# Kernel optimization log

Measured on AMD Instinct MI355X. Metric: run time of the kernel, lower is better.

The kernel has to match this reference:

```python
import jax, jax.numpy as jnp
import numpy as np
import math

N_EMBD = 1024
NUM_HEADS = 16
MAX_LEN = 2048
AUX = 256
B, T = 2, 2048


def setup_inputs() -> dict:
    key = jax.random.key(0)
    ks = jax.random.split(key, 16)
    s = 0.02
    C, A = N_EMBD, AUX
    inp = {
        "x": jax.random.normal(ks[0], (B, T, C), jnp.float32),
        "aux_x": jax.random.normal(ks[1], (B, T, A), jnp.float32),
        "Wq": s * jax.random.normal(ks[2], (C, C), jnp.float32),
        "bq": jnp.zeros((C,), jnp.float32),
        "Wk": s * jax.random.normal(ks[3], (C + A, C), jnp.float32),
        "bk": jnp.zeros((C,), jnp.float32),
        "Wv": s * jax.random.normal(ks[4], (C + A, C), jnp.float32),
        "bv": jnp.zeros((C,), jnp.float32),
        "Wo": s * jax.random.normal(ks[5], (C, C), jnp.float32),  # zero-init in source; randomized for a meaningful baseline
        "bo": jnp.zeros((C,), jnp.float32),
        "PEq": s * jax.random.normal(ks[6], (MAX_LEN, C), jnp.float32),
        "PEk": s * jax.random.normal(ks[7], (MAX_LEN, C), jnp.float32),
        "attn_mask": jax.random.bernoulli(ks[8], 0.9, (B, T, T)),
        "frame_indices": jax.random.randint(ks[9], (B, T), 0, MAX_LEN),
        "num_heads": NUM_HEADS,
    }
    return inp


def reference(x, aux_x, Wq, bq, Wk, bk, Wv, bv, Wo, bo, PEq, PEk, attn_mask, frame_indices, num_heads):
    Bx, Tx, C = x.shape
    H = num_heads
    hd = C // H
    x_aug = jnp.concatenate([x, aux_x], axis=2)  # [B,T,C+A]
    # QKV projections, split heads; PE added per (position, head) to q and k
    q = (x @ Wq + bq).reshape(Bx, Tx, H, hd) + PEq[frame_indices].reshape(Bx, Tx, H, hd)
    k = (x_aug @ Wk + bk).reshape(Bx, Tx, H, hd) + PEk[frame_indices].reshape(Bx, Tx, H, hd)
    v = (x_aug @ Wv + bv).reshape(Bx, Tx, H, hd)
    scale = 1.0 / math.sqrt(hd)
    scores = jnp.einsum("bqhd,bkhd->bhqk", q, k) * scale  # [B,H,T,T]
    scores = jnp.where(attn_mask[:, None, :, :], scores, -jnp.inf)
    attn = jax.nn.softmax(scores, axis=-1)  # fully-masked rows -> NaN
    out = jnp.einsum("bhqk,bkhd->bqhd", attn, v).reshape(Bx, Tx, C)
    out = jnp.nan_to_num(out, nan=0.0)
    return out @ Wo + bo
```

## Files before the change

### kernel.cpp

```cpp
#include <hip/hip_runtime.h>
#include <hip/hip_bf16.h>

typedef unsigned short u16;
typedef unsigned int u32;
typedef __attribute__((ext_vector_type(8))) short bf16x8;
typedef __attribute__((ext_vector_type(4))) float f32x4;

#define HD 64
#define NH 16
#define TT 2048
#define BB 2
#define CA 1280

__device__ __forceinline__ u16 bfu(float f) {
    u32 u = __builtin_bit_cast(u32, f);
    u32 r = u + 0x7fffu + ((u >> 16) & 1u);
    return (u16)(r >> 16);
}

__device__ __forceinline__ float ex2(float x) {
#if __has_builtin(__builtin_amdgcn_exp2f)
    return __builtin_amdgcn_exp2f(x);
#else
    return exp2f(x);
#endif
}

__device__ __forceinline__ void gload16(const void* g, void* l) {
    __builtin_amdgcn_global_load_lds(
        (const __attribute__((address_space(1))) unsigned int*)g,
        (__attribute__((address_space(3))) unsigned int*)l,
        16, 0, 0);
}

__global__ void build_xaug(const float* __restrict__ x, const float* __restrict__ aux,
                           u16* __restrict__ xa) {
    int i = blockIdx.x * 256 + threadIdx.x;
    int row = i / 320;
    int c4 = i - row * 320;
    float4 v;
    if (c4 < 256) v = ((const float4*)x)[row * 256 + c4];
    else          v = ((const float4*)aux)[row * 64 + (c4 - 256)];
    u16 o0 = bfu(v.x), o1 = bfu(v.y), o2 = bfu(v.z), o3 = bfu(v.w);
    ushort4 pk; pk.x = o0; pk.y = o1; pk.z = o2; pk.w = o3;
    ((ushort4*)xa)[i] = pk;
}

__global__ void wtrans_all(const float* __restrict__ Wq, const float* __restrict__ Wk,
                           const float* __restrict__ Wv, const float* __restrict__ Wo,
                           u16* __restrict__ WTall, u16* __restrict__ WTo) {
    int z = blockIdx.z;
    const float* src = (z == 0) ? Wq : (z == 1) ? Wk : (z == 2) ? Wv : Wo;
    u16* dst = (z == 3) ? WTo : WTall + (size_t)z * 1024 * 1280;
    int Ksrc = (z == 0 || z == 3) ? 1024 : 1280;
    int Kpad = (z == 3) ? 1024 : 1280;
    int kt = blockIdx.x * 32;
    if (kt >= Kpad) return;
    __shared__ float tile[32][33];
    int nt = blockIdx.y * 32;
    int r = threadIdx.x >> 5, c = threadIdx.x & 31;
    #pragma unroll
    for (int i = 0; i < 4; i++) {
        int k = kt + r + i * 8;
        tile[r + i * 8][c] = (k < Ksrc) ? src[(size_t)k * 1024 + nt + c] : 0.f;
    }
    __syncthreads();
    #pragma unroll
    for (int i = 0; i < 4; i++) {
        int n = nt + r + i * 8;
        dst[(size_t)n * Kpad + kt + c] = bfu(tile[c][r + i * 8]);
    }
}

__global__ void pack_mask(const unsigned char* __restrict__ m, u32* __restrict__ bits) {
    __shared__ u32 modeSh;
    if (threadIdx.x == 0) modeSh = 0;
    __syncthreads();
    const u32* wp = (const u32*)m;
    u32 local = 0;
    for (int j = threadIdx.x; j < 2048; j += 256) {
        u32 v = wp[j];
        if (v == 0x3f800000u) local |= 2u;
        else if (v > 1u) local |= 1u;
        if ((j & 1) && v != 0u) local |= 4u;
    }
    if (local) atomicOr(&modeSh, local);
    __syncthreads();
    u32 mode = modeSh;
    bool words32 = (mode & 2u) || (mode == 4u);
    bool bytes8 = !words32 && (mode & 1u);

    int i = blockIdx.x * 256 + threadIdx.x;
    size_t e0 = (size_t)i * 32;
    u32 r = 0;
    if (words32) {
        const uint4* q = (const uint4*)(wp + e0);
        #pragma unroll
        for (int j4 = 0; j4 < 8; j4++) {
            uint4 v = q[j4];
            if (v.x) r |= 1u << (j4 * 4 + 0);
            if (v.y) r |= 1u << (j4 * 4 + 1);
            if (v.z) r |= 1u << (j4 * 4 + 2);
            if (v.w) r |= 1u << (j4 * 4 + 3);
        }
    } else if (bytes8) {
        const unsigned char* p = m + e0;
        uint4 a = *(const uint4*)p;
        uint4 b = *(const uint4*)(p + 16);
        u32 words[8] = {a.x, a.y, a.z, a.w, b.x, b.y, b.z, b.w};
        #pragma unroll
        for (int jw = 0; jw < 8; jw++) {
            u32 x = words[jw];
            r |= ((x >> 0) & 1u) << (jw * 4 + 0);
            r |= ((x >> 8) & 1u) << (jw * 4 + 1);
            r |= ((x >> 16) & 1u) << (jw * 4 + 2);
            r |= ((x >> 24) & 1u) << (jw * 4 + 3);
        }
    } else {
        #pragma unroll 4
        for (int j = 0; j < 32; j++)
            if (wp[(e0 + j) * 2]) r |= 1u << j;
    }
    bits[i] = r;
}

template <int MODE>
__global__ __launch_bounds__(256, 3) void gemm_bt(
    const u16* __restrict__ A, const u16* __restrict__ Bt, int K,
    const float* __restrict__ biasq, const float* __restrict__ biask,
    const float* __restrict__ biasv, const float* __restrict__ PEq,
    const float* __restrict__ PEk, const int* __restrict__ fidx,
    u16* __restrict__ qo, u16* __restrict__ ko, u16* __restrict__ vto,
    float* __restrict__ fo, const float* __restrict__ bo) {
    __shared__ u16 As[128 * 64];
    __shared__ u16 Bs[128 * 64];
    const int tid = threadIdx.x, lane = tid & 63, w = tid >> 6;
    const int l15 = lane & 15, l4 = lane >> 4;
    const int wm = w >> 1, wn = w & 1;
    const int bm = blockIdx.x, bn = blockIdx.y;

    f32x4 acc[4][4] = {};

    const int srow = lane >> 3;
    const int schunk = (lane & 7) ^ srow;
    const u16* ag = A + (size_t)(bm * 128 + w * 32 + srow) * K + schunk * 8;
    const u16* bg = Bt + (size_t)(bn * 128 + w * 32 + srow) * K + schunk * 8;
    u16* asl = &As[(w * 32) * 64] + lane * 8;
    u16* bsl = &Bs[(w * 32) * 64] + lane * 8;

    for (int kt = 0; kt < K; kt += 64) {
        #pragma unroll
        for (int i = 0; i < 4; i++) {
            gload16(ag + (size_t)i * 8 * K + kt, asl + i * 8 * 64);
            gload16(bg + (size_t)i * 8 * K + kt, bsl + i * 8 * 64);
        }
        __syncthreads();
        #pragma unroll
        for (int ks = 0; ks < 2; ks++) {
            bf16x8 af[4], bfr[4];
            #pragma unroll
            for (int mi = 0; mi < 4; mi++) {
                int row = wm * 64 + mi * 16 + l15;
                af[mi] = *(const bf16x8*)&As[row * 64 + (((ks * 4 + l4) ^ (row & 7)) * 8)];
            }
            #pragma unroll
            for (int ni = 0; ni < 4; ni++) {
                int row = wn * 64 + ni * 16 + l15;
                bfr[ni] = *(const bf16x8*)&Bs[row * 64 + (((ks * 4 + l4) ^ (row & 7)) * 8)];
            }
            #pragma unroll
            for (int mi = 0; mi < 4; mi++)
                #pragma unroll
                for (int ni = 0; ni < 4; ni++)
                    acc[mi][ni] = __builtin_amdgcn_mfma_f32_16x16x32_bf16(
                        af[mi], bfr[ni], acc[mi][ni], 0, 0, 0);
        }
        __syncthreads();
    }

    if (MODE == 0) {
        int sec = bn >> 3;
        if (sec < 2) {
            const float* bias = sec ? biask : biasq;
            const float* PE   = sec ? PEk : PEq;
            u16* outp = sec ? ko : qo;
            float scl = sec ? 1.0f : 0.180336880111120419f;
            #pragma unroll
            for (int mi = 0; mi < 4; mi++) {
                #pragma unroll
                for (int r = 0; r < 4; r++) {
                    int m = bm * 128 + wm * 64 + mi * 16 + l4 * 4 + r;
                    int b = m >> 11, t = m & 2047;
                    int fi = fidx[m];
                    #pragma unroll
                    for (int ni = 0; ni < 4; ni++) {
                        int nn = (bn & 7) * 128 + wn * 64 + ni * 16 + l15;
                        float val = (acc[mi][ni][r] + bias[nn] + PE[(size_t)fi * 1024 + nn]) * scl;
                        outp[((size_t)(b * NH + (nn >> 6)) * TT + t) * HD + (nn & 63)] = bfu(val);
                    }
                }
            }
        } else {
            int b = bm >> 4;
            int t0 = (bm & 15) * 128 + wm * 64;
            #pragma unroll
            for (int ni = 0; ni < 4; ni++) {
                int nn = (bn - 16) * 128 + wn * 64 + ni * 16 + l15;
                float bvv = biasv[nn];
                int h = nn >> 6, d = nn & 63;
                u16* dst = vto + ((size_t)((b * NH + h) * HD + d)) * TT + t0;
                #pragma unroll
                for (int mi = 0; mi < 4; mi++) {
                    ushort4 pk;
                    pk.x = bfu(acc[mi][ni][0] + bvv);
                    pk.y = bfu(acc[mi][ni][1] + bvv);
                    pk.z = bfu(acc[mi][ni][2] + bvv);
                    pk.w = bfu(acc[mi][ni][3] + bvv);
                    *(ushort4*)(dst + mi * 16 + l4 * 4) = pk;
                }
            }
        }
    } else {
        #pragma unroll
        for (int mi = 0; mi < 4; mi++) {
            #pragma unroll
            for (int r = 0; r < 4; r++) {
                int m = bm * 128 + wm * 64 + mi * 16 + l4 * 4 + r;
                #pragma unroll
                for (int ni = 0; ni < 4; ni++) {
                    int ng = bn * 128 + wn * 64 + ni * 16 + l15;
                    fo[(size_t)m * 1024 + ng] = acc[mi][ni][r] + bo[ng];
                }
            }
        }
    }
}

__global__ __launch_bounds__(256, 4) void attn_fwd(
    const u16* __restrict__ Q, const u16* __restrict__ Kg,
    const u16* __restrict__ VT, const u32* __restrict__ mbits,
    u16* __restrict__ Og) {
    __shared__ u16 KPs[64 * 136];
    __shared__ u16 Vs[64 * 128];
    const int tid = threadIdx.x, lane = tid & 63, w = tid >> 6;
    const int l15 = lane & 15, l4 = lane >> 4;
    const int s_ = blockIdx.x;
    const int qt = (s_ >> 3) & 31;
    const int bh = (s_ & 7) * 4 + (s_ >> 8);
    const int b = bh >> 4;
    const size_t hoff = (size_t)bh * (TT * HD);

    bf16x8 qf[2];
    {
        int qbase = qt * 64 + w * 16;
        #pragma unroll
        for (int ks = 0; ks < 2; ks++)
            qf[ks] = *(const bf16x8*)&Q[hoff + (size_t)(qbase + l15) * HD + ks * 32 + l4 * 8];
    }

    bf16x8 ones;
    #pragma unroll
    for (int j = 0; j < 8; j++) ones[j] = (short)0x3F80;

    f32x4 po[4] = {};
    f32x4 pol = {};

    const int srow = lane >> 3;
    const int schunk = (lane & 7) ^ srow;
    const u16* kgl = Kg + hoff + (size_t)(w * 32 + srow) * HD + schunk * 8;
    u16* ksl = &KPs[(w * 32) * 64] + lane * 8;
    const size_t voff = (size_t)bh * (HD * TT);
    const size_t mbase = ((size_t)(b * TT + qt * 64 + w * 16 + l4 * 4)) * 64;
    const int shEven = 31 - l15, shOdd = 15 - l15;

    for (int kt = 0; kt < 16; kt++) {
        uint4 mb[4];
        #pragma unroll
        for (int r = 0; r < 4; r++)
            mb[r] = *(const uint4*)&mbits[mbase + (size_t)r * 64 + kt * 4];

        #pragma unroll
        for (int i = 0; i < 4; i++)
            gload16(kgl + (size_t)(kt * 128 + i * 8) * HD, ksl + i * 8 * 64);
        #pragma unroll
        for (int i = 0; i < 4; i++) {
            int d = w * 16 + i * 4 + l4;
            const u16* src = VT + voff + (size_t)d * TT + kt * 128 + ((l15 ^ (d & 15)) * 8);
            gload16(src, &Vs[(w * 16 + i * 4) * 128] + lane * 8);
        }
        __syncthreads();

        f32x4 s[8];
        __builtin_amdgcn_s_setprio(1);
        #pragma unroll
        for (int nt = 0; nt < 8; nt++) {
            int krow = nt * 16 + l15;
            bf16x8 kf0 = *(const bf16x8*)&KPs[krow * 64 + (((0 + l4) ^ (krow & 7)) * 8)];
            bf16x8 kf1 = *(const bf16x8*)&KPs[krow * 64 + (((4 + l4) ^ (krow & 7)) * 8)];
            f32x4 z = {0.f, 0.f, 0.f, 0.f};
            z = __builtin_amdgcn_mfma_f32_16x16x32_bf16(qf[0], kf0, z, 0, 0, 0);
            s[nt] = __builtin_amdgcn_mfma_f32_16x16x32_bf16(qf[1], kf1, z, 0, 0, 0);
        }
        __builtin_amdgcn_s_setprio(0);
        __syncthreads();

        #pragma unroll
        for (int r = 0; r < 4; r++) {
            u32 mw[4] = {mb[r].x, mb[r].y, mb[r].z, mb[r].w};
            int prow = w * 16 + l4 * 4 + r;
            u16* pw = &KPs[prow * 136 + l15];
            #pragma unroll
            for (int nt = 0; nt < 8; nt++) {
                u32 word = mw[nt >> 1];
                int sh = (nt & 1) ? shOdd : shEven;
                u32 ext = (u32)(((int)(word << sh)) >> 31);
                float p = ex2(s[nt][r]);
                u32 pb = __builtin_bit_cast(u32, p) & ext;
                pw[nt * 16] = (u16)(pb >> 16);
            }
        }

        bf16x8 pf[4];
        #pragma unroll
        for (int ks = 0; ks < 4; ks++)
            pf[ks] = *(const bf16x8*)&KPs[(w * 16 + l15) * 136 + ks * 32 + l4 * 8];
        __builtin_amdgcn_s_setprio(1);
        #pragma unroll
        for (int nto = 0; nto < 4; nto++) {
            #pragma unroll
            for (int ks = 0; ks < 4; ks++) {
                int d = nto * 16 + l15;
                bf16x8 vf = *(const bf16x8*)&Vs[d * 128 + (((ks * 4 + l4) ^ (d & 15)) * 8)];
                po[nto] = __builtin_amdgcn_mfma_f32_16x16x32_bf16(
                    pf[ks], vf, po[nto], 0, 0, 0);
            }
        }
        #pragma unroll
        for (int ks = 0; ks < 4; ks++)
            pol = __builtin_amdgcn_mfma_f32_16x16x32_bf16(pf[ks], ones, pol, 0, 0, 0);
        __builtin_amdgcn_s_setprio(0);
        __syncthreads();
    }

    int h = bh & 15;
    #pragma unroll
    for (int r = 0; r < 4; r++) {
        float lv = pol[r];
        float inv = (lv > 0.f) ? (1.f / lv) : 0.f;
        int t = qt * 64 + w * 16 + l4 * 4 + r;
        #pragma unroll
        for (int nto = 0; nto < 4; nto++)
            Og[((size_t)(b * TT + t)) * 1024 + h * 64 + nto * 16 + l15] =
                bfu(po[nto][r] * inv);
    }
}

extern "C" void kernel_launch(void* const* d_in, const int* in_sizes, int n_in,
                              void* d_out, int out_size, void* d_ws, size_t ws_size,
                              hipStream_t stream) {
    const float* x   = (const float*)d_in[0];
    const float* aux = (const float*)d_in[1];
    const float* Wq  = (const float*)d_in[2];
    const float* bq  = (const float*)d_in[3];
    const float* Wk  = (const float*)d_in[4];
    const float* bk  = (const float*)d_in[5];
    const float* Wv  = (const float*)d_in[6];
    const float* bv  = (const float*)d_in[7];
    const float* Wo  = (const float*)d_in[8];
    const float* bo  = (const float*)d_in[9];
    const float* PEq = (const float*)d_in[10];
    const float* PEk = (const float*)d_in[11];
    const unsigned char* mask = (const unsigned char*)d_in[12];
    const int* fidx  = (const int*)d_in[13];
    float* out = (float*)d_out;

    char* ws = (char*)d_ws;
    u16* XA    = (u16*)(ws + 0);
    u16* AttO  = (u16*)(ws + 0);
    u16* WTall = (u16*)(ws + 10485760);
    u16* WTo   = (u16*)(ws + 18350080);
    u16* Qb    = (u16*)(ws + 20447232);
    u16* Kb    = (u16*)(ws + 28835840);
    u16* VTb   = (u16*)(ws + 45613056);
    u32* MB    = (u32*)(ws + 54001664);

    build_xaug<<<5120, 256, 0, stream>>>(x, aux, XA);
    wtrans_all<<<dim3(40, 32, 4), 256, 0, stream>>>(Wq, Wk, Wv, Wo, WTall, WTo);
    pack_mask<<<1024, 256, 0, stream>>>(mask, MB);

    gemm_bt<0><<<dim3(32, 24), 256, 0, stream>>>(
        XA, WTall, 1280, bq, bk, bv, PEq, PEk, fidx, Qb, Kb, VTb, nullptr, nullptr);

    attn_fwd<<<1024, 256, 0, stream>>>(Qb, Kb, VTb, MB, AttO);

    gemm_bt<1><<<dim3(32, 8), 256, 0, stream>>>(
        AttO, WTo, 1024, nullptr, nullptr, nullptr, nullptr, nullptr, nullptr,
        nullptr, nullptr, nullptr, out, bo);
}
```

Measured before the change: 150.2 us.

## Use two waves per attention block, each computing 32 query rows

The attention kernel now runs 128 threads per block instead of 256. Each wave handles two 16-row query sub-tiles, so every K and V fragment read from shared memory feeds twice as many MFMAs. Each thread also does twice the global-to-LDS loads per tile. The aim is to halve LDS reads per MFMA and cut barrier cost, at the price of more registers per thread and fewer waves to hide latency (launch bounds 128,2).

```diff
diff --git a/kernel.cpp b/kernel.cpp
--- a/kernel.cpp
+++ b/kernel.cpp
@@ -236,7 +236,7 @@
     }
 }
 
-__global__ __launch_bounds__(256, 4) void attn_fwd(
+__global__ __launch_bounds__(128, 2) void attn_fwd(
     const u16* __restrict__ Q, const u16* __restrict__ Kg,
     const u16* __restrict__ VT, const u32* __restrict__ mbits,
     u16* __restrict__ Og) {
@@ -250,80 +250,90 @@
     const int b = bh >> 4;
     const size_t hoff = (size_t)bh * (TT * HD);
 
-    bf16x8 qf[2];
-    {
-        int qbase = qt * 64 + w * 16;
+    bf16x8 qf[2][2];
+    #pragma unroll
+    for (int mi = 0; mi < 2; mi++)
         #pragma unroll
         for (int ks = 0; ks < 2; ks++)
-            qf[ks] = *(const bf16x8*)&Q[hoff + (size_t)(qbase + l15) * HD + ks * 32 + l4 * 8];
-    }
+            qf[mi][ks] = *(const bf16x8*)&Q[hoff +
+                (size_t)(qt * 64 + w * 32 + mi * 16 + l15) * HD + ks * 32 + l4 * 8];
 
     bf16x8 ones;
     #pragma unroll
     for (int j = 0; j < 8; j++) ones[j] = (short)0x3F80;
 
-    f32x4 po[4] = {};
-    f32x4 pol = {};
+    f32x4 po[2][4] = {};
+    f32x4 pol[2] = {};
 
     const int srow = lane >> 3;
     const int schunk = (lane & 7) ^ srow;
-    const u16* kgl = Kg + hoff + (size_t)(w * 32 + srow) * HD + schunk * 8;
-    u16* ksl = &KPs[(w * 32) * 64] + lane * 8;
+    const u16* kgl = Kg + hoff + (size_t)(w * 64 + srow) * HD + schunk * 8;
+    u16* ksl = &KPs[(w * 64) * 64] + lane * 8;
     const size_t voff = (size_t)bh * (HD * TT);
-    const size_t mbase = ((size_t)(b * TT + qt * 64 + w * 16 + l4 * 4)) * 64;
+    const size_t mbase = ((size_t)(b * TT + qt * 64 + w * 32 + l4 * 4)) * 64;
     const int shEven = 31 - l15, shOdd = 15 - l15;
 
     for (int kt = 0; kt < 16; kt++) {
-        uint4 mb[4];
-        #pragma unroll
-        for (int r = 0; r < 4; r++)
-            mb[r] = *(const uint4*)&mbits[mbase + (size_t)r * 64 + kt * 4];
-
-        #pragma unroll
-        for (int i = 0; i < 4; i++)
+        uint4 mb[2][4];
+        #pragma unroll
+        for (int mi = 0; mi < 2; mi++)
+            #pragma unroll
+            for (int r = 0; r < 4; r++)
+                mb[mi][r] = *(const uint4*)&mbits[mbase + (size_t)(mi * 16 + r) * 64 + kt * 4];
+
+        #pragma unroll
+        for (int i = 0; i < 8; i++)
             gload16(kgl + (size_t)(kt * 128 + i * 8) * HD, ksl + i * 8 * 64);
         #pragma unroll
-        for (int i = 0; i < 4; i++) {
-            int d = w * 16 + i * 4 + l4;
+        for (int i = 0; i < 8; i++) {
+            int d = w * 32 + i * 4 + l4;
             const u16* src = VT + voff + (size_t)d * TT + kt * 128 + ((l15 ^ (d & 15)) * 8);
-            gload16(src, &Vs[(w * 16 + i * 4) * 128] + lane * 8);
+            gload16(src, &Vs[(w * 32 + i * 4) * 128] + lane * 8);
         }
         __syncthreads();
 
-        f32x4 s[8];
+        f32x4 s[2][8];
         __builtin_amdgcn_s_setprio(1);
         #pragma unroll
         for (int nt = 0; nt < 8; nt++) {
             int krow = nt * 16 + l15;
             bf16x8 kf0 = *(const bf16x8*)&KPs[krow * 64 + (((0 + l4) ^ (krow & 7)) * 8)];
             bf16x8 kf1 = *(const bf16x8*)&KPs[krow * 64 + (((4 + l4) ^ (krow & 7)) * 8)];
-            f32x4 z = {0.f, 0.f, 0.f, 0.f};
-            z = __builtin_amdgcn_mfma_f32_16x16x32_bf16(qf[0], kf0, z, 0, 0, 0);
-            s[nt] = __builtin_amdgcn_mfma_f32_16x16x32_bf16(qf[1], kf1, z, 0, 0, 0);
+            #pragma unroll
+            for (int mi = 0; mi < 2; mi++) {
+                f32x4 z = {0.f, 0.f, 0.f, 0.f};
+                z = __builtin_amdgcn_mfma_f32_16x16x32_bf16(qf[mi][0], kf0, z, 0, 0, 0);
+                s[mi][nt] = __builtin_amdgcn_mfma_f32_16x16x32_bf16(qf[mi][1], kf1, z, 0, 0, 0);
+            }
         }
         __builtin_amdgcn_s_setprio(0);
         __syncthreads();
 
         #pragma unroll
-        for (int r = 0; r < 4; r++) {
-            u32 mw[4] = {mb[r].x, mb[r].y, mb[r].z, mb[r].w};
-            int prow = w * 16 + l4 * 4 + r;
-            u16* pw = &KPs[prow * 136 + l15];
-            #pragma unroll
-            for (int nt = 0; nt < 8; nt++) {
-                u32 word = mw[nt >> 1];
-                int sh = (nt & 1) ? shOdd : shEven;
-                u32 ext = (u32)(((int)(word << sh)) >> 31);
-                float p = ex2(s[nt][r]);
-                u32 pb = __builtin_bit_cast(u32, p) & ext;
-                pw[nt * 16] = (u16)(pb >> 16);
-            }
-        }
-
-        bf16x8 pf[4];
-        #pragma unroll
-        for (int ks = 0; ks < 4; ks++)
-            pf[ks] = *(const bf16x8*)&KPs[(w * 16 + l15) * 136 + ks * 32 + l4 * 8];
+        for (int mi = 0; mi < 2; mi++) {
+            #pragma unroll
+            for (int r = 0; r < 4; r++) {
+                u32 mw[4] = {mb[mi][r].x, mb[mi][r].y, mb[mi][r].z, mb[mi][r].w};
+                int prow = w * 32 + mi * 16 + l4 * 4 + r;
+                u16* pw = &KPs[prow * 136 + l15];
+                #pragma unroll
+                for (int nt = 0; nt < 8; nt++) {
+                    u32 word = mw[nt >> 1];
+                    int sh = (nt & 1) ? shOdd : shEven;
+                    u32 ext = (u32)(((int)(word << sh)) >> 31);
+                    float p = ex2(s[mi][nt][r]);
+                    u32 pb = __builtin_bit_cast(u32, p) & ext;
+                    pw[nt * 16] = (u16)(pb >> 16);
+                }
+            }
+        }
+
+        bf16x8 pf[2][4];
+        #pragma unroll
+        for (int mi = 0; mi < 2; mi++)
+            #pragma unroll
+            for (int ks = 0; ks < 4; ks++)
+                pf[mi][ks] = *(const bf16x8*)&KPs[(w * 32 + mi * 16 + l15) * 136 + ks * 32 + l4 * 8];
         __builtin_amdgcn_s_setprio(1);
         #pragma unroll
         for (int nto = 0; nto < 4; nto++) {
@@ -331,27 +341,34 @@
             for (int ks = 0; ks < 4; ks++) {
                 int d = nto * 16 + l15;
                 bf16x8 vf = *(const bf16x8*)&Vs[d * 128 + (((ks * 4 + l4) ^ (d & 15)) * 8)];
-                po[nto] = __builtin_amdgcn_mfma_f32_16x16x32_bf16(
-                    pf[ks], vf, po[nto], 0, 0, 0);
-            }
-        }
-        #pragma unroll
-        for (int ks = 0; ks < 4; ks++)
-            pol = __builtin_amdgcn_mfma_f32_16x16x32_bf16(pf[ks], ones, pol, 0, 0, 0);
+                #pragma unroll
+                for (int mi = 0; mi < 2; mi++)
+                    po[mi][nto] = __builtin_amdgcn_mfma_f32_16x16x32_bf16(
+                        pf[mi][ks], vf, po[mi][nto], 0, 0, 0);
+            }
+        }
+        #pragma unroll
+        for (int mi = 0; mi < 2; mi++)
+            #pragma unroll
+            for (int ks = 0; ks < 4; ks++)
+                pol[mi] = __builtin_amdgcn_mfma_f32_16x16x32_bf16(pf[mi][ks], ones, pol[mi], 0, 0, 0);
         __builtin_amdgcn_s_setprio(0);
         __syncthreads();
     }
 
     int h = bh & 15;
     #pragma unroll
-    for (int r = 0; r < 4; r++) {
-        float lv = pol[r];
-        float inv = (lv > 0.f) ? (1.f / lv) : 0.f;
-        int t = qt * 64 + w * 16 + l4 * 4 + r;
-        #pragma unroll
-        for (int nto = 0; nto < 4; nto++)
-            Og[((size_t)(b * TT + t)) * 1024 + h * 64 + nto * 16 + l15] =
-                bfu(po[nto][r] * inv);
+    for (int mi = 0; mi < 2; mi++) {
+        #pragma unroll
+        for (int r = 0; r < 4; r++) {
+            float lv = pol[mi][r];
+            float inv = (lv > 0.f) ? (1.f / lv) : 0.f;
+            int t = qt * 64 + w * 32 + mi * 16 + l4 * 4 + r;
+            #pragma unroll
+            for (int nto = 0; nto < 4; nto++)
+                Og[((size_t)(b * TT + t)) * 1024 + h * 64 + nto * 16 + l15] =
+                    bfu(po[mi][nto][r] * inv);
+        }
     }
 }
 
@@ -391,7 +408,7 @@
     gemm_bt<0><<<dim3(32, 24), 256, 0, stream>>>(
         XA, WTall, 1280, bq, bk, bv, PEq, PEk, fidx, Qb, Kb, VTb, nullptr, nullptr);
 
-    attn_fwd<<<1024, 256, 0, stream>>>(Qb, Kb, VTb, MB, AttO);
+    attn_fwd<<<1024, 128, 0, stream>>>(Qb, Kb, VTb, MB, AttO);
 
     gemm_bt<1><<<dim3(32, 8), 256, 0, stream>>>(
         AttO, WTo, 1024, nullptr, nullptr, nullptr, nullptr, nullptr, nullptr,
```

Result: no change. 153.1 us (+1.9%).
